# Optimization experiments

Hardware: AMD Instinct MI355X
Metric: run time of the kernel (lower is better)

The kernel has to match this reference:

```python
import jax, jax.numpy as jnp
import numpy as np
from jax import lax

N_EMBD = 4096
N_EXPERTS = 64


def setup_inputs() -> dict:
    key = jax.random.key(0)
    kx, kw = jax.random.split(key)
    x = jax.random.normal(kx, (4, 4096, N_EMBD), dtype=jnp.float32)
    # nn.Linear(n_embd, n_experts, bias=False) -> weight shape [n_experts, n_embd]
    W = jax.random.normal(kw, (N_EXPERTS, N_EMBD), dtype=jnp.float32) * (1.0 / np.sqrt(N_EMBD))
    return {"x": x, "W": W}


def reference(x, W):
    # logits = x @ W^T : [B, S, n_experts]
    logits = jnp.einsum('bsd,ed->bse', x, W)
    topk_vals, topk_idx = lax.top_k(logits, 2)  # [B, S, 2]
    gates = jax.nn.softmax(topk_vals, axis=-1)  # softmax over just the top-2 values
    return (topk_idx, gates)
```

## Files before the change

### kernel.cpp

```cpp
#include <hip/hip_runtime.h>
#include <math.h>

#define N_EMBD    4096
#define N_EXPERTS 64
#define N_TOKENS  16384
#define TAU       1e-3f

typedef __attribute__((ext_vector_type(8))) short bf16x8;
typedef __attribute__((ext_vector_type(4))) float f32x4;
typedef __attribute__((ext_vector_type(4))) unsigned u32x4;

#define MFMA16 __builtin_amdgcn_mfma_f32_16x16x32_bf16

struct hl_pair { unsigned h, l; };

__device__ __forceinline__ hl_pair split_pair(float f0, float f1) {
    unsigned u0 = __builtin_bit_cast(unsigned, f0);
    unsigned u1 = __builtin_bit_cast(unsigned, f1);
    unsigned r0 = u0 + 0x7FFFu + ((u0 >> 16) & 1u);
    unsigned r1 = u1 + 0x7FFFu + ((u1 >> 16) & 1u);
    hl_pair p;
    p.h = (r0 >> 16) | (r1 & 0xFFFF0000u);
    float h0 = __builtin_bit_cast(float, r0 & 0xFFFF0000u);
    float h1 = __builtin_bit_cast(float, r1 & 0xFFFF0000u);
    float l0 = f0 - h0;
    float l1 = f1 - h1;
    unsigned v0 = __builtin_bit_cast(unsigned, l0);
    unsigned v1 = __builtin_bit_cast(unsigned, l1);
    unsigned s0 = v0 + 0x7FFFu + ((v0 >> 16) & 1u);
    unsigned s1 = v1 + 0x7FFFu + ((v1 >> 16) & 1u);
    p.l = (s0 >> 16) | (s1 & 0xFFFF0000u);
    return p;
}

__global__ void w_pack_bf16(const float* __restrict__ W,
                            uint4* __restrict__ Bpack,
                            int* __restrict__ flags) {
    int tid = blockIdx.x * blockDim.x + threadIdx.x;
    if (tid == 0) flags[0] = 0;
    int lane = tid & 63;
    int nt   = (tid >> 6) & 3;
    int ks   = tid >> 8;
    int e = nt * 16 + (lane & 15);
    int k = ks * 32 + ((lane >> 4) << 3);
    const float* src = W + (size_t)e * N_EMBD + k;
    uint4 hp, lp;
    hl_pair p0 = split_pair(src[0], src[1]);
    hl_pair p1 = split_pair(src[2], src[3]);
    hl_pair p2 = split_pair(src[4], src[5]);
    hl_pair p3 = split_pair(src[6], src[7]);
    hp.x = p0.h; lp.x = p0.l;
    hp.y = p1.h; lp.y = p1.l;
    hp.z = p2.h; lp.z = p2.l;
    hp.w = p3.h; lp.w = p3.l;
    size_t F = (size_t)ks * 8 + nt * 2;
    Bpack[F * 64 + lane]       = hp;
    Bpack[(F + 1) * 64 + lane] = lp;
}

__device__ __forceinline__ void split_tile(f32x4 A0, f32x4 A1,
                                           bf16x8& ah, bf16x8& al) {
    u32x4 hu, lu;
    hl_pair p;
    p = split_pair(A0.x, A0.y); hu.x = p.h; lu.x = p.l;
    p = split_pair(A0.z, A0.w); hu.y = p.h; lu.y = p.l;
    p = split_pair(A1.x, A1.y); hu.z = p.h; lu.z = p.l;
    p = split_pair(A1.z, A1.w); hu.w = p.h; lu.w = p.l;
    ah = __builtin_bit_cast(bf16x8, hu);
    al = __builtin_bit_cast(bf16x8, lu);
}

__device__ __forceinline__ void step2(
        f32x4 A0, f32x4 A1, f32x4 A2, f32x4 A3,
        uint4 B0, uint4 B1, uint4 B2, uint4 B3,
        uint4 B4, uint4 B5, uint4 B6, uint4 B7,
        f32x4& c00, f32x4& c01, f32x4& c02, f32x4& c03,
        f32x4& c10, f32x4& c11, f32x4& c12, f32x4& c13) {
    bf16x8 ah0, al0, ah1, al1;
    split_tile(A0, A1, ah0, al0);
    split_tile(A2, A3, ah1, al1);
    bf16x8 bh, bl;
    bh = __builtin_bit_cast(bf16x8, B0); bl = __builtin_bit_cast(bf16x8, B1);
    c00 = MFMA16(ah0, bh, c00, 0, 0, 0);
    c00 = MFMA16(ah0, bl, c00, 0, 0, 0);
    c00 = MFMA16(al0, bh, c00, 0, 0, 0);
    c10 = MFMA16(ah1, bh, c10, 0, 0, 0);
    c10 = MFMA16(ah1, bl, c10, 0, 0, 0);
    c10 = MFMA16(al1, bh, c10, 0, 0, 0);
    bh = __builtin_bit_cast(bf16x8, B2); bl = __builtin_bit_cast(bf16x8, B3);
    c01 = MFMA16(ah0, bh, c01, 0, 0, 0);
    c01 = MFMA16(ah0, bl, c01, 0, 0, 0);
    c01 = MFMA16(al0, bh, c01, 0, 0, 0);
    c11 = MFMA16(ah1, bh, c11, 0, 0, 0);
    c11 = MFMA16(ah1, bl, c11, 0, 0, 0);
    c11 = MFMA16(al1, bh, c11, 0, 0, 0);
    bh = __builtin_bit_cast(bf16x8, B4); bl = __builtin_bit_cast(bf16x8, B5);
    c02 = MFMA16(ah0, bh, c02, 0, 0, 0);
    c02 = MFMA16(ah0, bl, c02, 0, 0, 0);
    c02 = MFMA16(al0, bh, c02, 0, 0, 0);
    c12 = MFMA16(ah1, bh, c12, 0, 0, 0);
    c12 = MFMA16(ah1, bl, c12, 0, 0, 0);
    c12 = MFMA16(al1, bh, c12, 0, 0, 0);
    bh = __builtin_bit_cast(bf16x8, B6); bl = __builtin_bit_cast(bf16x8, B7);
    c03 = MFMA16(ah0, bh, c03, 0, 0, 0);
    c03 = MFMA16(ah0, bl, c03, 0, 0, 0);
    c03 = MFMA16(al0, bh, c03, 0, 0, 0);
    c13 = MFMA16(ah1, bh, c13, 0, 0, 0);
    c13 = MFMA16(ah1, bl, c13, 0, 0, 0);
    c13 = MFMA16(al1, bh, c13, 0, 0, 0);
}

__global__ __launch_bounds__(256, 2) void router_fused(
        const float* __restrict__ x,
        const uint4* __restrict__ Bpack,
        float* __restrict__ out,
        int* __restrict__ flags) {
    __shared__ float red[4][32][64];
    const int lane = threadIdx.x & 63;
    const int kq   = threadIdx.x >> 6;
    const int tok0 = blockIdx.x * 32;

    const f32x4* pa0 = (const f32x4*)x
        + (size_t)(tok0 + (lane & 15)) * (N_EMBD / 4)
        + kq * 256 + ((lane >> 4) << 1);
    const f32x4* pa1 = pa0 + (size_t)16 * (N_EMBD / 4);
    const uint4* pb = Bpack + (size_t)kq * 16384 + lane;

    f32x4 c00 = {0.f,0.f,0.f,0.f}, c01 = {0.f,0.f,0.f,0.f};
    f32x4 c02 = {0.f,0.f,0.f,0.f}, c03 = {0.f,0.f,0.f,0.f};
    f32x4 c10 = {0.f,0.f,0.f,0.f}, c11 = {0.f,0.f,0.f,0.f};
    f32x4 c12 = {0.f,0.f,0.f,0.f}, c13 = {0.f,0.f,0.f,0.f};

    uint4 ba0, ba1, ba2, ba3, ba4, ba5, ba6, ba7;
    uint4 bb0, bb1, bb2, bb3, bb4, bb5, bb6, bb7;
    f32x4 aa0, aa1, aa2, aa3, ab0, ab1, ab2, ab3;

#define LOADB(P, s) { const uint4* _q = pb + (size_t)(s) * 512;               \
    P##0 = _q[0];   P##1 = _q[64];  P##2 = _q[128]; P##3 = _q[192];           \
    P##4 = _q[256]; P##5 = _q[320]; P##6 = _q[384]; P##7 = _q[448]; }
#define LOADA(P, s) {                                                          \
    P##0 = __builtin_nontemporal_load(pa0 + (s) * 8);                          \
    P##1 = __builtin_nontemporal_load(pa0 + (s) * 8 + 1);                      \
    P##2 = __builtin_nontemporal_load(pa1 + (s) * 8);                          \
    P##3 = __builtin_nontemporal_load(pa1 + (s) * 8 + 1); }

    LOADA(aa, 0); LOADB(ba, 0);
    for (int s = 0; s < 32; s += 2) {
        LOADA(ab, s + 1); LOADB(bb, s + 1);
        step2(aa0, aa1, aa2, aa3, ba0, ba1, ba2, ba3, ba4, ba5, ba6, ba7,
              c00, c01, c02, c03, c10, c11, c12, c13);
        if (s < 30) { LOADA(aa, s + 2); LOADB(ba, s + 2); }
        step2(ab0, ab1, ab2, ab3, bb0, bb1, bb2, bb3, bb4, bb5, bb6, bb7,
              c00, c01, c02, c03, c10, c11, c12, c13);
    }
#undef LOADB
#undef LOADA

    const int l15 = lane & 15;
    const int rb  = (lane >> 4) << 2;
#pragma unroll
    for (int j = 0; j < 4; ++j) {
        red[kq][rb + j][l15]      = c00[j];
        red[kq][rb + j][16 + l15] = c01[j];
        red[kq][rb + j][32 + l15] = c02[j];
        red[kq][rb + j][48 + l15] = c03[j];
        red[kq][16 + rb + j][l15]      = c10[j];
        red[kq][16 + rb + j][16 + l15] = c11[j];
        red[kq][16 + rb + j][32 + l15] = c12[j];
        red[kq][16 + rb + j][48 + l15] = c13[j];
    }
    __syncthreads();

    for (int tt = 0; tt < 8; ++tt) {
        const int t = kq * 8 + tt;
        float v = red[0][t][lane] + red[1][t][lane]
                + red[2][t][lane] + red[3][t][lane];

        float m1 = v; int i1 = lane;
#pragma unroll
        for (int off = 32; off; off >>= 1) {
            float ov = __shfl_xor(m1, off); int oi = __shfl_xor(i1, off);
            if (ov > m1 || (ov == m1 && oi < i1)) { m1 = ov; i1 = oi; }
        }
        float m2 = (lane == i1) ? -INFINITY : v; int i2 = lane;
#pragma unroll
        for (int off = 32; off; off >>= 1) {
            float ov = __shfl_xor(m2, off); int oi = __shfl_xor(i2, off);
            if (ov > m2 || (ov == m2 && oi < i2)) { m2 = ov; i2 = oi; }
        }
        float m3 = (lane == i1 || lane == i2) ? -INFINITY : v;
#pragma unroll
        for (int off = 32; off; off >>= 1)
            m3 = fmaxf(m3, __shfl_xor(m3, off));

        if (lane == 0) {
            const int tok = tok0 + t;
            float e2  = __expf(m2 - m1);
            float inv = 1.0f / (1.0f + e2);
            float2 idx = make_float2((float)i1, (float)i2);
            float2 gts = make_float2(inv, e2 * inv);
            *(float2*)(out + 2 * tok) = idx;
            *(float2*)(out + 2 * N_TOKENS + 2 * tok) = gts;
            if ((m1 - m2 < TAU) || (m2 - m3 < TAU)) {
                int p = atomicAdd(flags, 1);
                if (p < N_TOKENS) flags[1 + p] = tok;
            }
        }
    }
}

__global__ __launch_bounds__(256) void refine(const float* __restrict__ x,
                                              const float* __restrict__ W,
                                              const int* __restrict__ flags,
                                              float* __restrict__ out) {
    __shared__ double redd[64];
    const int lane = threadIdx.x & 63;
    const int wv   = threadIdx.x >> 6;
    int cnt = flags[0];
    if (cnt > N_TOKENS) cnt = N_TOKENS;

    for (int i = blockIdx.x; i < cnt; i += gridDim.x) {
        const int tok = flags[1 + i];
        const float4* xr4 = (const float4*)(x + (size_t)tok * N_EMBD);
#pragma unroll
        for (int ee = 0; ee < 16; ++ee) {
            const int e = wv * 16 + ee;
            const float4* wr = (const float4*)(W + (size_t)e * N_EMBD);
            double acc = 0.0;
#pragma unroll 4
            for (int c = 0; c < 16; ++c) {
                float4 xv = xr4[c * 64 + lane];
                float4 wq = wr[c * 64 + lane];
                acc += (double)xv.x * wq.x + (double)xv.y * wq.y
                     + (double)xv.z * wq.z + (double)xv.w * wq.w;
            }
#pragma unroll
            for (int off = 32; off; off >>= 1)
                acc += __shfl_xor(acc, off);
            if (lane == 0) redd[e] = acc;
        }
        __syncthreads();
        if (wv == 0) {
            double v = redd[lane];
            double m1 = v; int i1 = lane;
#pragma unroll
            for (int off = 32; off; off >>= 1) {
                double ov = __shfl_xor(m1, off); int oi = __shfl_xor(i1, off);
                if (ov > m1 || (ov == m1 && oi < i1)) { m1 = ov; i1 = oi; }
            }
            double m2 = (lane == i1) ? -INFINITY : v; int i2 = lane;
#pragma unroll
            for (int off = 32; off; off >>= 1) {
                double ov = __shfl_xor(m2, off); int oi = __shfl_xor(i2, off);
                if (ov > m2 || (ov == m2 && oi < i2)) { m2 = ov; i2 = oi; }
            }
            if (lane == 0) {
                double e2  = exp(m2 - m1);
                double inv = 1.0 / (1.0 + e2);
                out[2 * tok + 0] = (float)i1;
                out[2 * tok + 1] = (float)i2;
                out[2 * N_TOKENS + 2 * tok + 0] = (float)inv;
                out[2 * N_TOKENS + 2 * tok + 1] = (float)(e2 * inv);
            }
        }
        __syncthreads();
    }
}

extern "C" void kernel_launch(void* const* d_in, const int* in_sizes, int n_in,
                              void* d_out, int out_size, void* d_ws, size_t ws_size,
                              hipStream_t stream) {
    const float* x = (const float*)d_in[0];
    const float* W = (const float*)d_in[1];
    float* out = (float*)d_out;

    uint4* Bpack = (uint4*)d_ws;
    int*   flags = (int*)((char*)d_ws + (2u << 20));

    w_pack_bf16 <<<128, 256, 0, stream>>>(W, Bpack, flags);
    router_fused<<<N_TOKENS / 32, 256, 0, stream>>>(x, Bpack, out, flags);
    refine      <<<128, 256, 0, stream>>>(x, W, flags, out);
}
```

Measured before the change: 131.6 us.

## Restructure router GEMM to stage split A tiles in LDS with per-wave expert tiles

The router kernel used to split K across four waves, each holding a 32-token tile in registers and reducing partial sums through shared memory. Now each block handles 16 tokens. The x tile is loaded cooperatively, split into bf16 hi/lo once, and stored in swizzled LDS, and each wave computes the full K range for its own 16 experts. This removes the cross-wave K reduction, splits each x element only once, and shrinks register use so occupancy can reach 3 blocks. In exchange there are two barriers per K tile and much more B traffic per token, because Bpack is re-read by twice as many blocks.

```diff
diff --git a/kernel.cpp b/kernel.cpp
--- a/kernel.cpp
+++ b/kernel.cpp
@@ -5,10 +5,12 @@
 #define N_EXPERTS 64
 #define N_TOKENS  16384
 #define TAU       1e-3f
+#define BM        16
+#define BK        128
+#define NTILES    (N_EMBD / BK)
 
 typedef __attribute__((ext_vector_type(8))) short bf16x8;
 typedef __attribute__((ext_vector_type(4))) float f32x4;
-typedef __attribute__((ext_vector_type(4))) unsigned u32x4;
 
 #define MFMA16 __builtin_amdgcn_mfma_f32_16x16x32_bf16
 
@@ -58,123 +60,79 @@
     Bpack[(F + 1) * 64 + lane] = lp;
 }
 
-__device__ __forceinline__ void split_tile(f32x4 A0, f32x4 A1,
-                                           bf16x8& ah, bf16x8& al) {
-    u32x4 hu, lu;
-    hl_pair p;
-    p = split_pair(A0.x, A0.y); hu.x = p.h; lu.x = p.l;
-    p = split_pair(A0.z, A0.w); hu.y = p.h; lu.y = p.l;
-    p = split_pair(A1.x, A1.y); hu.z = p.h; lu.z = p.l;
-    p = split_pair(A1.z, A1.w); hu.w = p.h; lu.w = p.l;
-    ah = __builtin_bit_cast(bf16x8, hu);
-    al = __builtin_bit_cast(bf16x8, lu);
-}
-
-__device__ __forceinline__ void step2(
-        f32x4 A0, f32x4 A1, f32x4 A2, f32x4 A3,
-        uint4 B0, uint4 B1, uint4 B2, uint4 B3,
-        uint4 B4, uint4 B5, uint4 B6, uint4 B7,
-        f32x4& c00, f32x4& c01, f32x4& c02, f32x4& c03,
-        f32x4& c10, f32x4& c11, f32x4& c12, f32x4& c13) {
-    bf16x8 ah0, al0, ah1, al1;
-    split_tile(A0, A1, ah0, al0);
-    split_tile(A2, A3, ah1, al1);
-    bf16x8 bh, bl;
-    bh = __builtin_bit_cast(bf16x8, B0); bl = __builtin_bit_cast(bf16x8, B1);
-    c00 = MFMA16(ah0, bh, c00, 0, 0, 0);
-    c00 = MFMA16(ah0, bl, c00, 0, 0, 0);
-    c00 = MFMA16(al0, bh, c00, 0, 0, 0);
-    c10 = MFMA16(ah1, bh, c10, 0, 0, 0);
-    c10 = MFMA16(ah1, bl, c10, 0, 0, 0);
-    c10 = MFMA16(al1, bh, c10, 0, 0, 0);
-    bh = __builtin_bit_cast(bf16x8, B2); bl = __builtin_bit_cast(bf16x8, B3);
-    c01 = MFMA16(ah0, bh, c01, 0, 0, 0);
-    c01 = MFMA16(ah0, bl, c01, 0, 0, 0);
-    c01 = MFMA16(al0, bh, c01, 0, 0, 0);
-    c11 = MFMA16(ah1, bh, c11, 0, 0, 0);
-    c11 = MFMA16(ah1, bl, c11, 0, 0, 0);
-    c11 = MFMA16(al1, bh, c11, 0, 0, 0);
-    bh = __builtin_bit_cast(bf16x8, B4); bl = __builtin_bit_cast(bf16x8, B5);
-    c02 = MFMA16(ah0, bh, c02, 0, 0, 0);
-    c02 = MFMA16(ah0, bl, c02, 0, 0, 0);
-    c02 = MFMA16(al0, bh, c02, 0, 0, 0);
-    c12 = MFMA16(ah1, bh, c12, 0, 0, 0);
-    c12 = MFMA16(ah1, bl, c12, 0, 0, 0);
-    c12 = MFMA16(al1, bh, c12, 0, 0, 0);
-    bh = __builtin_bit_cast(bf16x8, B6); bl = __builtin_bit_cast(bf16x8, B7);
-    c03 = MFMA16(ah0, bh, c03, 0, 0, 0);
-    c03 = MFMA16(ah0, bl, c03, 0, 0, 0);
-    c03 = MFMA16(al0, bh, c03, 0, 0, 0);
-    c13 = MFMA16(ah1, bh, c13, 0, 0, 0);
-    c13 = MFMA16(ah1, bl, c13, 0, 0, 0);
-    c13 = MFMA16(al1, bh, c13, 0, 0, 0);
-}
-
-__global__ __launch_bounds__(256, 2) void router_fused(
+__device__ __forceinline__ void store_split(char* ldsA, int off, f32x4 v) {
+    hl_pair p01 = split_pair(v.x, v.y);
+    hl_pair p23 = split_pair(v.z, v.w);
+    uint2 hw, lw;
+    hw.x = p01.h; hw.y = p23.h;
+    lw.x = p01.l; lw.y = p23.l;
+    *(uint2*)(ldsA + off)        = hw;
+    *(uint2*)(ldsA + off + 4096) = lw;
+}
+
+__global__ __launch_bounds__(256, 3) void router_fused(
         const float* __restrict__ x,
         const uint4* __restrict__ Bpack,
         float* __restrict__ out,
         int* __restrict__ flags) {
-    __shared__ float red[4][32][64];
-    const int lane = threadIdx.x & 63;
-    const int kq   = threadIdx.x >> 6;
-    const int tok0 = blockIdx.x * 32;
-
-    const f32x4* pa0 = (const f32x4*)x
-        + (size_t)(tok0 + (lane & 15)) * (N_EMBD / 4)
-        + kq * 256 + ((lane >> 4) << 1);
-    const f32x4* pa1 = pa0 + (size_t)16 * (N_EMBD / 4);
-    const uint4* pb = Bpack + (size_t)kq * 16384 + lane;
-
-    f32x4 c00 = {0.f,0.f,0.f,0.f}, c01 = {0.f,0.f,0.f,0.f};
-    f32x4 c02 = {0.f,0.f,0.f,0.f}, c03 = {0.f,0.f,0.f,0.f};
-    f32x4 c10 = {0.f,0.f,0.f,0.f}, c11 = {0.f,0.f,0.f,0.f};
-    f32x4 c12 = {0.f,0.f,0.f,0.f}, c13 = {0.f,0.f,0.f,0.f};
-
-    uint4 ba0, ba1, ba2, ba3, ba4, ba5, ba6, ba7;
-    uint4 bb0, bb1, bb2, bb3, bb4, bb5, bb6, bb7;
-    f32x4 aa0, aa1, aa2, aa3, ab0, ab1, ab2, ab3;
-
-#define LOADB(P, s) { const uint4* _q = pb + (size_t)(s) * 512;               \
-    P##0 = _q[0];   P##1 = _q[64];  P##2 = _q[128]; P##3 = _q[192];           \
-    P##4 = _q[256]; P##5 = _q[320]; P##6 = _q[384]; P##7 = _q[448]; }
-#define LOADA(P, s) {                                                          \
-    P##0 = __builtin_nontemporal_load(pa0 + (s) * 8);                          \
-    P##1 = __builtin_nontemporal_load(pa0 + (s) * 8 + 1);                      \
-    P##2 = __builtin_nontemporal_load(pa1 + (s) * 8);                          \
-    P##3 = __builtin_nontemporal_load(pa1 + (s) * 8 + 1); }
-
-    LOADA(aa, 0); LOADB(ba, 0);
-    for (int s = 0; s < 32; s += 2) {
-        LOADA(ab, s + 1); LOADB(bb, s + 1);
-        step2(aa0, aa1, aa2, aa3, ba0, ba1, ba2, ba3, ba4, ba5, ba6, ba7,
-              c00, c01, c02, c03, c10, c11, c12, c13);
-        if (s < 30) { LOADA(aa, s + 2); LOADB(ba, s + 2); }
-        step2(ab0, ab1, ab2, ab3, bb0, bb1, bb2, bb3, bb4, bb5, bb6, bb7,
-              c00, c01, c02, c03, c10, c11, c12, c13);
+    __shared__ __align__(16) char ldsA[8192];
+    __shared__ float red[BM][64];
+
+    const int tid  = threadIdx.x;
+    const int lane = tid & 63;
+    const int w    = tid >> 6;
+    const int tok0 = blockIdx.x * BM;
+
+    const int k4   = tid & 31;
+    const int row0 = tid >> 5;
+    const f32x4* g0 = (const f32x4*)x + (size_t)(tok0 + row0) * (N_EMBD / 4) + k4;
+    const f32x4* g1 = g0 + 8 * (N_EMBD / 4);
+    const int swz = (row0 & 7) << 4;
+    const int wo0 = ((row0    ) * 256 + k4 * 8) ^ swz;
+    const int wo1 = ((row0 + 8) * 256 + k4 * 8) ^ swz;
+
+    const int l15 = lane & 15, l16 = lane >> 4;
+    const int ro_base = l15 * 256 + l16 * 16;
+    const int swz_r   = (l15 & 7) << 4;
+
+    f32x4 acc = {0.f, 0.f, 0.f, 0.f};
+
+    f32x4 r0 = g0[0];
+    f32x4 r1 = g1[0];
+    for (int t = 0; t < NTILES; ++t) {
+        __syncthreads();
+        store_split(ldsA, wo0, r0);
+        store_split(ldsA, wo1, r1);
+        if (t + 1 < NTILES) {
+            r0 = g0[(t + 1) * (BK / 4)];
+            r1 = g1[(t + 1) * (BK / 4)];
+        }
+        __syncthreads();
+#pragma unroll
+        for (int ksl = 0; ksl < 4; ++ksl) {
+            const uint4* bq = Bpack + ((size_t)(t * 4 + ksl) * 8 + w * 2) * 64 + lane;
+            uint4 bhq = bq[0];
+            uint4 blq = bq[64];
+            const int off = (ro_base + ksl * 64) ^ swz_r;
+            bf16x8 ah = *(const bf16x8*)(ldsA + off);
+            bf16x8 al = *(const bf16x8*)(ldsA + off + 4096);
+            bf16x8 bh = __builtin_bit_cast(bf16x8, bhq);
+            bf16x8 bl = __builtin_bit_cast(bf16x8, blq);
+            acc = MFMA16(ah, bh, acc, 0, 0, 0);
+            acc = MFMA16(ah, bl, acc, 0, 0, 0);
+            acc = MFMA16(al, bh, acc, 0, 0, 0);
+        }
     }
-#undef LOADB
-#undef LOADA
-
-    const int l15 = lane & 15;
-    const int rb  = (lane >> 4) << 2;
-#pragma unroll
-    for (int j = 0; j < 4; ++j) {
-        red[kq][rb + j][l15]      = c00[j];
-        red[kq][rb + j][16 + l15] = c01[j];
-        red[kq][rb + j][32 + l15] = c02[j];
-        red[kq][rb + j][48 + l15] = c03[j];
-        red[kq][16 + rb + j][l15]      = c10[j];
-        red[kq][16 + rb + j][16 + l15] = c11[j];
-        red[kq][16 + rb + j][32 + l15] = c12[j];
-        red[kq][16 + rb + j][48 + l15] = c13[j];
-    }
+
+    const int rb = l16 << 2;
+#pragma unroll
+    for (int j = 0; j < 4; ++j)
+        red[rb + j][w * 16 + l15] = acc[j];
     __syncthreads();
 
-    for (int tt = 0; tt < 8; ++tt) {
-        const int t = kq * 8 + tt;
-        float v = red[0][t][lane] + red[1][t][lane]
-                + red[2][t][lane] + red[3][t][lane];
+    for (int tt = 0; tt < 4; ++tt) {
+        const int t = w * 4 + tt;
+        float v = red[t][lane];
 
         float m1 = v; int i1 = lane;
 #pragma unroll
@@ -278,6 +236,6 @@
     int*   flags = (int*)((char*)d_ws + (2u << 20));
 
     w_pack_bf16 <<<128, 256, 0, stream>>>(W, Bpack, flags);
-    router_fused<<<N_TOKENS / 32, 256, 0, stream>>>(x, Bpack, out, flags);
+    router_fused<<<N_TOKENS / BM, 256, 0, stream>>>(x, Bpack, out, flags);
     refine      <<<128, 256, 0, stream>>>(x, W, flags, out);
 }
```

Result: faster. 110.8 us (-15.8%).

## Split-K router GEMM into 8 slices with separate finalize reduction kernel

Applied to the files above, without the earlier changes.

Replaces the fused router kernel, which reduced four K-quarters through shared memory, with a split-K GEMM. Eight waves, each owning one K-slice of 512, write partial logits to a global workspace, and a separate finalize kernel sums the slices and does the top-2, softmax and flagging. The aim is more independent waves, higher occupancy and shorter per-wave K loops to better saturate memory bandwidth on the 256 MB activation read. In exchange it adds a 32 MB partial-logit write and read-back, an extra kernel launch, drops the nontemporal hints and the B-register double buffering, and moves the flags and workspace offsets.

```diff
diff --git a/kernel.cpp b/kernel.cpp
--- a/kernel.cpp
+++ b/kernel.cpp
@@ -5,6 +5,8 @@
 #define N_EXPERTS 64
 #define N_TOKENS  16384
 #define TAU       1e-3f
+#define KS        8
+#define KSTEPS    16
 
 typedef __attribute__((ext_vector_type(8))) short bf16x8;
 typedef __attribute__((ext_vector_type(4))) float f32x4;
@@ -110,101 +112,108 @@
     c13 = MFMA16(al1, bh, c13, 0, 0, 0);
 }
 
-__global__ __launch_bounds__(256, 2) void router_fused(
+__global__ __launch_bounds__(256, 4) void router_gemm(
         const float* __restrict__ x,
         const uint4* __restrict__ Bpack,
-        float* __restrict__ out,
-        int* __restrict__ flags) {
-    __shared__ float red[4][32][64];
-    const int lane = threadIdx.x & 63;
-    const int kq   = threadIdx.x >> 6;
-    const int tok0 = blockIdx.x * 32;
-
-    const f32x4* pa0 = (const f32x4*)x
-        + (size_t)(tok0 + (lane & 15)) * (N_EMBD / 4)
-        + kq * 256 + ((lane >> 4) << 1);
+        float* __restrict__ partial) {
+    const int tid  = threadIdx.x;
+    const int lane = tid & 63;
+    const int wid  = blockIdx.x * 4 + (tid >> 6);
+    const int kq   = wid & 7;
+    const int tg   = wid >> 3;
+    const int tok0 = tg * 32;
+    const int l15 = lane & 15, l16 = lane >> 4;
+
+    const f32x4* pa0 = (const f32x4*)x + (size_t)(tok0 + l15) * (N_EMBD / 4)
+                     + kq * (N_EMBD / 4 / KS) + l16 * 2;
     const f32x4* pa1 = pa0 + (size_t)16 * (N_EMBD / 4);
-    const uint4* pb = Bpack + (size_t)kq * 16384 + lane;
+    const uint4* pb = Bpack + ((size_t)kq * KSTEPS * 8) * 64 + lane;
 
     f32x4 c00 = {0.f,0.f,0.f,0.f}, c01 = {0.f,0.f,0.f,0.f};
     f32x4 c02 = {0.f,0.f,0.f,0.f}, c03 = {0.f,0.f,0.f,0.f};
     f32x4 c10 = {0.f,0.f,0.f,0.f}, c11 = {0.f,0.f,0.f,0.f};
     f32x4 c12 = {0.f,0.f,0.f,0.f}, c13 = {0.f,0.f,0.f,0.f};
 
-    uint4 ba0, ba1, ba2, ba3, ba4, ba5, ba6, ba7;
-    uint4 bb0, bb1, bb2, bb3, bb4, bb5, bb6, bb7;
     f32x4 aa0, aa1, aa2, aa3, ab0, ab1, ab2, ab3;
 
-#define LOADB(P, s) { const uint4* _q = pb + (size_t)(s) * 512;               \
-    P##0 = _q[0];   P##1 = _q[64];  P##2 = _q[128]; P##3 = _q[192];           \
-    P##4 = _q[256]; P##5 = _q[320]; P##6 = _q[384]; P##7 = _q[448]; }
-#define LOADA(P, s) {                                                          \
-    P##0 = __builtin_nontemporal_load(pa0 + (s) * 8);                          \
-    P##1 = __builtin_nontemporal_load(pa0 + (s) * 8 + 1);                      \
-    P##2 = __builtin_nontemporal_load(pa1 + (s) * 8);                          \
-    P##3 = __builtin_nontemporal_load(pa1 + (s) * 8 + 1); }
-
-    LOADA(aa, 0); LOADB(ba, 0);
-    for (int s = 0; s < 32; s += 2) {
-        LOADA(ab, s + 1); LOADB(bb, s + 1);
-        step2(aa0, aa1, aa2, aa3, ba0, ba1, ba2, ba3, ba4, ba5, ba6, ba7,
-              c00, c01, c02, c03, c10, c11, c12, c13);
-        if (s < 30) { LOADA(aa, s + 2); LOADB(ba, s + 2); }
-        step2(ab0, ab1, ab2, ab3, bb0, bb1, bb2, bb3, bb4, bb5, bb6, bb7,
-              c00, c01, c02, c03, c10, c11, c12, c13);
-    }
-#undef LOADB
+#define LOADA(P, s) { P##0 = pa0[(s) * 8]; P##1 = pa0[(s) * 8 + 1];            \
+                      P##2 = pa1[(s) * 8]; P##3 = pa1[(s) * 8 + 1]; }
+
+    LOADA(aa, 0);
+    for (int s = 0; s < KSTEPS; s += 2) {
+        LOADA(ab, s + 1);
+        {
+            const uint4* q = pb + (size_t)s * 512;
+            uint4 B0 = q[0],   B1 = q[64],  B2 = q[128], B3 = q[192];
+            uint4 B4 = q[256], B5 = q[320], B6 = q[384], B7 = q[448];
+            step2(aa0, aa1, aa2, aa3, B0, B1, B2, B3, B4, B5, B6, B7,
+                  c00, c01, c02, c03, c10, c11, c12, c13);
+        }
+        if (s + 2 < KSTEPS) LOADA(aa, s + 2);
+        {
+            const uint4* q = pb + (size_t)(s + 1) * 512;
+            uint4 B0 = q[0],   B1 = q[64],  B2 = q[128], B3 = q[192];
+            uint4 B4 = q[256], B5 = q[320], B6 = q[384], B7 = q[448];
+            step2(ab0, ab1, ab2, ab3, B0, B1, B2, B3, B4, B5, B6, B7,
+                  c00, c01, c02, c03, c10, c11, c12, c13);
+        }
+    }
 #undef LOADA
 
-    const int l15 = lane & 15;
-    const int rb  = (lane >> 4) << 2;
+    float* po = partial + ((size_t)kq * N_TOKENS + tok0) * 64 + l15;
 #pragma unroll
     for (int j = 0; j < 4; ++j) {
-        red[kq][rb + j][l15]      = c00[j];
-        red[kq][rb + j][16 + l15] = c01[j];
-        red[kq][rb + j][32 + l15] = c02[j];
-        red[kq][rb + j][48 + l15] = c03[j];
-        red[kq][16 + rb + j][l15]      = c10[j];
-        red[kq][16 + rb + j][16 + l15] = c11[j];
-        red[kq][16 + rb + j][32 + l15] = c12[j];
-        red[kq][16 + rb + j][48 + l15] = c13[j];
-    }
-    __syncthreads();
-
-    for (int tt = 0; tt < 8; ++tt) {
-        const int t = kq * 8 + tt;
-        float v = red[0][t][lane] + red[1][t][lane]
-                + red[2][t][lane] + red[3][t][lane];
-
-        float m1 = v; int i1 = lane;
-#pragma unroll
-        for (int off = 32; off; off >>= 1) {
-            float ov = __shfl_xor(m1, off); int oi = __shfl_xor(i1, off);
-            if (ov > m1 || (ov == m1 && oi < i1)) { m1 = ov; i1 = oi; }
-        }
-        float m2 = (lane == i1) ? -INFINITY : v; int i2 = lane;
-#pragma unroll
-        for (int off = 32; off; off >>= 1) {
-            float ov = __shfl_xor(m2, off); int oi = __shfl_xor(i2, off);
-            if (ov > m2 || (ov == m2 && oi < i2)) { m2 = ov; i2 = oi; }
-        }
-        float m3 = (lane == i1 || lane == i2) ? -INFINITY : v;
-#pragma unroll
-        for (int off = 32; off; off >>= 1)
-            m3 = fmaxf(m3, __shfl_xor(m3, off));
-
-        if (lane == 0) {
-            const int tok = tok0 + t;
-            float e2  = __expf(m2 - m1);
-            float inv = 1.0f / (1.0f + e2);
-            float2 idx = make_float2((float)i1, (float)i2);
-            float2 gts = make_float2(inv, e2 * inv);
-            *(float2*)(out + 2 * tok) = idx;
-            *(float2*)(out + 2 * N_TOKENS + 2 * tok) = gts;
-            if ((m1 - m2 < TAU) || (m2 - m3 < TAU)) {
-                int p = atomicAdd(flags, 1);
-                if (p < N_TOKENS) flags[1 + p] = tok;
-            }
+        size_t r0 = (size_t)(l16 * 4 + j) * 64;
+        size_t r1 = (size_t)(16 + l16 * 4 + j) * 64;
+        po[r0 +  0] = c00[j];
+        po[r0 + 16] = c01[j];
+        po[r0 + 32] = c02[j];
+        po[r0 + 48] = c03[j];
+        po[r1 +  0] = c10[j];
+        po[r1 + 16] = c11[j];
+        po[r1 + 32] = c12[j];
+        po[r1 + 48] = c13[j];
+    }
+}
+
+__global__ void finalize(const float* __restrict__ partial,
+                         float* __restrict__ out,
+                         int* __restrict__ flags) {
+    const int lane = threadIdx.x & 63;
+    const int tok  = blockIdx.x * 4 + (threadIdx.x >> 6);
+
+    float v = 0.0f;
+#pragma unroll
+    for (int q = 0; q < KS; ++q)
+        v += partial[((size_t)q * N_TOKENS + tok) * 64 + lane];
+
+    float m1 = v; int i1 = lane;
+#pragma unroll
+    for (int off = 32; off; off >>= 1) {
+        float ov = __shfl_xor(m1, off); int oi = __shfl_xor(i1, off);
+        if (ov > m1 || (ov == m1 && oi < i1)) { m1 = ov; i1 = oi; }
+    }
+    float m2 = (lane == i1) ? -INFINITY : v; int i2 = lane;
+#pragma unroll
+    for (int off = 32; off; off >>= 1) {
+        float ov = __shfl_xor(m2, off); int oi = __shfl_xor(i2, off);
+        if (ov > m2 || (ov == m2 && oi < i2)) { m2 = ov; i2 = oi; }
+    }
+    float m3 = (lane == i1 || lane == i2) ? -INFINITY : v;
+#pragma unroll
+    for (int off = 32; off; off >>= 1)
+        m3 = fmaxf(m3, __shfl_xor(m3, off));
+
+    if (lane == 0) {
+        float e2  = __expf(m2 - m1);
+        float inv = 1.0f / (1.0f + e2);
+        float2 idx = make_float2((float)i1, (float)i2);
+        float2 gts = make_float2(inv, e2 * inv);
+        *(float2*)(out + 2 * tok) = idx;
+        *(float2*)(out + 2 * N_TOKENS + 2 * tok) = gts;
+        if ((m1 - m2 < TAU) || (m2 - m3 < TAU)) {
+            int p = atomicAdd(flags, 1);
+            if (p < N_TOKENS) flags[1 + p] = tok;
         }
     }
 }
@@ -274,10 +283,12 @@
     const float* W = (const float*)d_in[1];
     float* out = (float*)d_out;
 
-    uint4* Bpack = (uint4*)d_ws;
-    int*   flags = (int*)((char*)d_ws + (2u << 20));
-
-    w_pack_bf16 <<<128, 256, 0, stream>>>(W, Bpack, flags);
-    router_fused<<<N_TOKENS / 32, 256, 0, stream>>>(x, Bpack, out, flags);
-    refine      <<<128, 256, 0, stream>>>(x, W, flags, out);
-}
+    uint4* Bpack   = (uint4*)d_ws;
+    int*   flags   = (int*)((char*)d_ws + (1u << 20));
+    float* partial = (float*)((char*)d_ws + (2u << 20));
+
+    w_pack_bf16<<<128, 256, 0, stream>>>(W, Bpack, flags);
+    router_gemm<<<(N_TOKENS / 32) * KS / 4, 256, 0, stream>>>(x, Bpack, partial);
+    finalize   <<<N_TOKENS / 4, 256, 0, stream>>>(partial, out, flags);
+    refine     <<<128, 256, 0, stream>>>(x, W, flags, out);
+}
```

New measurement: 125.0 us. 5.0% less time.
